# Kernel optimization log

Hardware: AMD Instinct MI355X
Metric: run time of the kernel (lower is better)

The kernel has to match this reference:

```python
import jax, jax.numpy as jnp
import numpy as np

EMBEDDING_SIZE = 50
MAX_DOCUMENT_LENGTH = 100
MAX_LABEL = 15
VOCAB = 200000
HID = 1024
BATCH = 4096


def setup_inputs() -> dict:
    key = jax.random.key(0)
    ks = jax.random.split(key, 8)
    x = jax.random.randint(ks[0], (BATCH, MAX_DOCUMENT_LENGTH), 0, VOCAB)
    emb_table = jax.random.normal(ks[1], (VOCAB, EMBEDDING_SIZE), jnp.float32) * 0.05
    # Keras GRUCell (reset_after=True): kernel [E,3H], recurrent_kernel [H,3H],
    # bias [2,3H] split into input bias and recurrent bias; gate order z, r, h.
    kernel = jax.random.normal(ks[2], (EMBEDDING_SIZE, 3 * HID), jnp.float32) * (1.0 / np.sqrt(EMBEDDING_SIZE))
    rec_kernel = jax.random.normal(ks[3], (HID, 3 * HID), jnp.float32) * (1.0 / np.sqrt(HID))
    bias_i = jnp.zeros((3 * HID,), jnp.float32)
    bias_r = jnp.zeros((3 * HID,), jnp.float32)
    Wd = jax.random.normal(ks[4], (HID, MAX_LABEL), jnp.float32) * (1.0 / np.sqrt(HID))
    bd = jnp.zeros((MAX_LABEL,), jnp.float32)
    return {"x": x, "drop_rate": 0, "emb_table": emb_table, "kernel": kernel,
            "rec_kernel": rec_kernel, "bias_i": bias_i, "bias_r": bias_r,
            "Wd": Wd, "bd": bd}


def _gru_scan(emb, kernel, rec_kernel, bias_i, bias_r):
    # emb: [B,T,E] -> time-major [T,B,E]
    emb_t = jnp.transpose(emb, (1, 0, 2))
    B = emb.shape[0]
    h0 = jnp.zeros((B, HID), emb.dtype)

    def step(h, x_t):
        xp = x_t @ kernel + bias_i            # [B,3H]
        hp = h @ rec_kernel + bias_r          # [B,3H]
        xz, xr, xh = jnp.split(xp, 3, axis=-1)
        hz, hr, hh = jnp.split(hp, 3, axis=-1)
        z = jax.nn.sigmoid(xz + hz)
        r = jax.nn.sigmoid(xr + hr)
        hcand = jnp.tanh(xh + r * hh)
        h_new = z * h + (1.0 - z) * hcand
        return h_new, None

    h_last, _ = jax.lax.scan(step, h0, emb_t)
    return h_last


def reference(x, drop_rate, emb_table, kernel, rec_kernel, bias_i, bias_r, Wd, bd):
    emb = emb_table[x]                         # [B,T,E]
    encoding = _gru_scan(emb, kernel, rec_kernel, bias_i, bias_r)  # [B,H]
    if drop_rate > 0:                          # drop_rate is a static Python int
        keep = 1.0 - float(drop_rate)
        mask = jax.random.bernoulli(jax.random.key(1), keep, encoding.shape)
        encoding = jnp.where(mask, encoding / keep, 0.0)
    logits = encoding @ Wd + bd                # [B,15]
    return logits
```

## Files before the change

kernel.cpp:

```cpp
#include <hip/hip_runtime.h>
#include <stdint.h>

#define H_DIM   1024
#define G3      3072
#define EMB     50
#define TSTEPS  100
#define NB      4096
#define NLABEL  15

typedef __bf16 bf16x8 __attribute__((ext_vector_type(8)));
typedef float  f32x4  __attribute__((ext_vector_type(4)));
typedef int    i32x4  __attribute__((ext_vector_type(4)));

__device__ inline uint16_t f2bf(float f) {
  uint32_t u = __builtin_bit_cast(uint32_t, f);
  u += 0x7FFFu + ((u >> 16) & 1u);
  return (uint16_t)(u >> 16);
}

__device__ inline void gld16(const void* g, void* l) {
  __builtin_amdgcn_global_load_lds(
      (const __attribute__((address_space(1))) uint32_t*)g,
      (__attribute__((address_space(3))) uint32_t*)l, 16, 0, 0);
}

#define VM(n) do { asm volatile("s_waitcnt vmcnt(" #n ")" ::: "memory"); \
                   __builtin_amdgcn_sched_barrier(0); } while (0)
#define LGKM0() do { asm volatile("s_waitcnt lgkmcnt(0)" ::: "memory"); \
                     __builtin_amdgcn_sched_barrier(0); } while (0)
#define BARF() do { __builtin_amdgcn_s_barrier(); \
                    asm volatile("" ::: "memory"); } while (0)
#define GLDB(dst, addr, OFF) \
  asm volatile("global_load_dwordx4 %0, %1, off offset:" OFF \
               : "=&v"(dst) : "v"(addr) : "memory")


__global__ __launch_bounds__(256) void prep_recT(const float* __restrict__ rec,
                                                 uint16_t* __restrict__ recT) {
  __shared__ uint16_t st[64][72];
  const int n0 = blockIdx.x * 64;
  const int k0 = blockIdx.y * 64;
  const int tid = threadIdx.x;
#pragma unroll
  for (int i = 0; i < 16; ++i) {
    int idx = tid + i * 256;
    int r = idx >> 6;
    int c = idx & 63;
    st[c][r] = f2bf(rec[(size_t)(k0 + r) * G3 + n0 + c]);
  }
  __syncthreads();
#pragma unroll
  for (int i = 0; i < 16; ++i) {
    int idx = tid + i * 256;
    int r = idx >> 6;
    int c = idx & 63;
    recT[(size_t)(n0 + r) * H_DIM + k0 + c] = st[r][c];
  }
}

__global__ __launch_bounds__(256) void prep_kerT(const float* __restrict__ ker,
                                                 uint16_t* __restrict__ kerT) {
  int n = blockIdx.x * 4 + (threadIdx.x >> 6);
  int k = threadIdx.x & 63;
  float v = (k < EMB) ? ker[(size_t)k * G3 + n] : 0.f;
  kerT[(size_t)n * 64 + k] = f2bf(v);
}

__global__ __launch_bounds__(256) void prep_pack(const uint16_t* __restrict__ recT,
                                                 const uint16_t* __restrict__ kerT,
                                                 uint16_t* __restrict__ Bpk) {
  int cid = blockIdx.x * 256 + threadIdx.x;
  int lane = cid & 63;
  int r = cid >> 6;
  int ks = r & 1; r >>= 1;
  int nf = r & 1; r >>= 1;
  int wn = r & 1; r >>= 1;
  int g  = r % 3; r /= 3;
  int kt = r % 17;
  int colblk = r / 17;
  int n  = g * H_DIM + colblk * 64 + wn * 32 + nf * 16 + (lane & 15);
  int kk = ks * 32 + (lane >> 4) * 8;
  const uint16_t* src = (kt < 16) ? recT + (size_t)n * H_DIM + kt * 64 + kk
                                  : kerT + (size_t)n * 64 + kk;
  *reinterpret_cast<i32x4*>(Bpk + (size_t)cid * 8) =
      *reinterpret_cast<const i32x4*>(src);
}

__global__ __launch_bounds__(256) void prep_embt(const int* __restrict__ x,
                                                 const float* __restrict__ tab,
                                                 uint16_t* __restrict__ embt) {
  int idx = blockIdx.x * 256 + threadIdx.x;
  int g = idx >> 5;
  int p = idx & 31;
  int t = g >> 12;
  int b = g & 4095;
  int row = x[b * TSTEPS + t];
  float2 v;
  if (p < 25) v = *reinterpret_cast<const float2*>(tab + (size_t)row * EMB + 2 * p);
  else { v.x = 0.f; v.y = 0.f; }
  uint32_t packed = (uint32_t)f2bf(v.x) | ((uint32_t)f2bf(v.y) << 16);
  *reinterpret_cast<uint32_t*>(embt + (size_t)g * 64 + 2 * p) = packed;
}

__global__ __launch_bounds__(256, 2) void gru_step_kernel(
    const uint16_t* __restrict__ hb_prev,
    float* __restrict__ hf,
    uint16_t* __restrict__ hb_next,
    const uint16_t* __restrict__ Bpk,
    const uint16_t* __restrict__ embt,
    const float* __restrict__ bias_i,
    const float* __restrict__ bias_r) {
  __shared__ __align__(16) uint16_t sA2[2][128 * 64];

  const int tid  = threadIdx.x;
  const int lane = tid & 63;
  const int wid  = tid >> 6;
  const int wm   = wid >> 1;
  const int wn   = wid & 1;
  const int bid  = blockIdx.x;
  const int xk = bid & 7, slot = bid >> 3;
  const int rowblk = (xk >> 1) * 8 + (slot >> 3);
  const int colblk = (xk & 1) * 8 + (slot & 7);
  const int r0 = rowblk * 128;
  const int j0 = colblk * 64;

  const int swz8 = 8 * ((lane & 7) ^ (lane >> 3));

  bf16x8 af[4][2];
  i32x4  bfv[3][2][2];
  f32x4 accZ[4][2], accR[4][2], accH[4][2], accX[4][2];
#pragma unroll
  for (int m = 0; m < 4; ++m)
#pragma unroll
    for (int n = 0; n < 2; ++n) {
      accZ[m][n] = (f32x4){0.f, 0.f, 0.f, 0.f};
      accR[m][n] = (f32x4){0.f, 0.f, 0.f, 0.f};
      accH[m][n] = (f32x4){0.f, 0.f, 0.f, 0.f};
      accX[m][n] = (f32x4){0.f, 0.f, 0.f, 0.f};
    }

  const uint16_t* pB[3];
#pragma unroll
  for (int g = 0; g < 3; ++g)
    pB[g] = Bpk + (size_t)colblk * 17 * 12288 + g * 4096 + wn * 2048 + lane * 8;

  auto stageA = [&](int t) {
    const int abuf = t & 1;
#pragma unroll
    for (int i = 0; i < 4; ++i) {
      int chunk = wid * 4 + i;
      int row = chunk * 8 + (lane >> 3);
      const uint16_t* src = (t < 16)
          ? hb_prev + (size_t)(r0 + row) * H_DIM + t * 64 + swz8
          : embt + (size_t)(r0 + row) * 64 + swz8;
      gld16(src, &sA2[abuf][(chunk * 64 + lane) * 8]);
    }
  };
  auto readA = [&](int t) {
    const int abuf = t & 1;
#pragma unroll
    for (int ks = 0; ks < 2; ++ks) {
      const int colswz = (ks * 32 + (lane >> 4) * 8) ^ ((lane & 7) << 3);
#pragma unroll
      for (int mf = 0; mf < 4; ++mf)
        af[mf][ks] = *reinterpret_cast<const bf16x8*>(
            &sA2[abuf][(wm * 64 + mf * 16 + (lane & 15)) * 64 + colswz]);
    }
  };

#define ISSUE_BG(g) do { \
    GLDB(bfv[g][0][0], pB[g], "0");    GLDB(bfv[g][0][1], pB[g], "1024"); \
    GLDB(bfv[g][1][0], pB[g], "2048"); GLDB(bfv[g][1][1], pB[g], "3072"); \
  } while (0)
#define MFG(g, ACC) do { \
    __builtin_amdgcn_s_setprio(1); \
    _Pragma("unroll") for (int ks = 0; ks < 2; ++ks) \
    _Pragma("unroll") for (int nf = 0; nf < 2; ++nf) \
    _Pragma("unroll") for (int mf = 0; mf < 4; ++mf) \
      ACC[mf][nf] = __builtin_amdgcn_mfma_f32_16x16x32_bf16( \
          af[mf][ks], __builtin_bit_cast(bf16x8, bfv[g][nf][ks]), \
          ACC[mf][nf], 0, 0, 0); \
    __builtin_amdgcn_s_setprio(0); \
  } while (0)
#define ADV_B() do { _Pragma("unroll") \
    for (int g = 0; g < 3; ++g) pB[g] += 12288; } while (0)

  stageA(0); stageA(1);
  ISSUE_BG(0); ISSUE_BG(1); ISSUE_BG(2);
  ADV_B();
  VM(12);
  BARF();
  readA(0);

  for (int t = 0; t < 15; ++t) {
    stageA(t + 2);
    VM(12);
    MFG(0, accZ); ISSUE_BG(0);
    VM(12);
    MFG(1, accR); ISSUE_BG(1);
    VM(12);
    MFG(2, accH); ISSUE_BG(2);
    ADV_B();
    readA(t + 1);
    LGKM0();
    VM(12);
    BARF();
  }

  VM(8);  MFG(0, accZ); ISSUE_BG(0);
  VM(8);  MFG(1, accR); ISSUE_BG(1);
  VM(8);  MFG(2, accH); ISSUE_BG(2);
  readA(16);
  LGKM0();
  VM(8);  MFG(0, accZ);
  VM(4);  MFG(1, accR);
  VM(0);  MFG(2, accX);

#undef ISSUE_BG
#undef MFG
#undef ADV_B

#pragma unroll
  for (int nf = 0; nf < 2; ++nf) {
    int col = j0 + wn * 32 + nf * 16 + (lane & 15);
    float b_z = bias_i[col] + bias_r[col];
    float b_r = bias_i[H_DIM + col] + bias_r[H_DIM + col];
    float bih = bias_i[2 * H_DIM + col];
    float brh = bias_r[2 * H_DIM + col];
#pragma unroll
    for (int mf = 0; mf < 4; ++mf) {
#pragma unroll
      for (int q = 0; q < 4; ++q) {
        int row = r0 + wm * 64 + mf * 16 + (lane >> 4) * 4 + q;
        float z  = 1.f / (1.f + __expf(-(accZ[mf][nf][q] + b_z)));
        float rr = 1.f / (1.f + __expf(-(accR[mf][nf][q] + b_r)));
        float pre = accX[mf][nf][q] + bih + rr * (accH[mf][nf][q] + brh);
        float hc  = 2.f / (1.f + __expf(-2.f * pre)) - 1.f;
        size_t idx = (size_t)row * H_DIM + col;
        float hold = hf[idx];
        float hnew = z * hold + (1.f - z) * hc;
        hf[idx] = hnew;
        hb_next[idx] = f2bf(hnew);
      }
    }
  }
}

__global__ __launch_bounds__(64) void logits_kernel(const float* __restrict__ hf,
                                                    const float* __restrict__ Wd,
                                                    const float* __restrict__ bd,
                                                    float* __restrict__ out) {
  int b = blockIdx.x;
  int l = threadIdx.x;
  float p[NLABEL];
#pragma unroll
  for (int o = 0; o < NLABEL; ++o) p[o] = 0.f;
  for (int kb = 0; kb < 16; ++kb) {
    int k = kb * 64 + l;
    float hv = hf[(size_t)b * H_DIM + k];
#pragma unroll
    for (int o = 0; o < NLABEL; ++o) p[o] += hv * Wd[k * NLABEL + o];
  }
#pragma unroll
  for (int o = 0; o < NLABEL; ++o) {
#pragma unroll
    for (int s = 32; s; s >>= 1) p[o] += __shfl_xor(p[o], s);
  }
  if (l == 0) {
#pragma unroll
    for (int o = 0; o < NLABEL; ++o) out[(size_t)b * NLABEL + o] = p[o] + bd[o];
  }
}

extern "C" void kernel_launch(void* const* d_in, const int* in_sizes, int n_in,
                              void* d_out, int out_size, void* d_ws, size_t ws_size,
                              hipStream_t stream) {
  const int*   x          = (const int*)d_in[0];
  const float* emb_table  = (const float*)d_in[2];
  const float* kernel_w   = (const float*)d_in[3];
  const float* rec_kernel = (const float*)d_in[4];
  const float* bias_i     = (const float*)d_in[5];
  const float* bias_r     = (const float*)d_in[6];
  const float* Wd         = (const float*)d_in[7];
  const float* bd         = (const float*)d_in[8];
  float* out = (float*)d_out;

  char* ws = (char*)d_ws;
  size_t off = 0;
  auto alloc = [&](size_t bytes) {
    char* p = ws + off;
    off += (bytes + 255) & ~(size_t)255;
    return p;
  };
  float*    hf   = (float*)alloc((size_t)NB * H_DIM * 4);
  uint16_t* hb0  = (uint16_t*)alloc((size_t)NB * H_DIM * 2);
  uint16_t* hb1  = (uint16_t*)alloc((size_t)NB * H_DIM * 2);
  uint16_t* recT = (uint16_t*)alloc((size_t)G3 * H_DIM * 2);
  uint16_t* kerT = (uint16_t*)alloc((size_t)G3 * 64 * 2);
  uint16_t* embt = (uint16_t*)alloc((size_t)TSTEPS * NB * 64 * 2);
  uint16_t* Bpk  = (uint16_t*)alloc((size_t)16 * 17 * 12288 * 2);
  if (off > ws_size) return;

  hipMemsetAsync(hf, 0, (size_t)NB * H_DIM * 4, stream);
  hipMemsetAsync(hb0, 0, (size_t)NB * H_DIM * 2, stream);

  prep_recT<<<dim3(G3 / 64, H_DIM / 64), 256, 0, stream>>>(rec_kernel, recT);
  prep_kerT<<<G3 / 4, 256, 0, stream>>>(kernel_w, kerT);
  prep_pack<<<1632, 256, 0, stream>>>(recT, kerT, Bpk);
  prep_embt<<<TSTEPS * NB * 32 / 256, 256, 0, stream>>>(x, emb_table, embt);

  uint16_t* hb[2] = {hb0, hb1};
  for (int t = 0; t < TSTEPS; ++t) {
    gru_step_kernel<<<512, 256, 0, stream>>>(
        hb[t & 1], hf, hb[(t + 1) & 1], Bpk,
        embt + (size_t)t * NB * 64, bias_i, bias_r);
  }
  logits_kernel<<<NB, 64, 0, stream>>>(hf, Wd, bd, out);
}
```

Baseline: 3.151 ms.

## Deepen GRU step pipeline to triple-buffered A tiles and double-buffered B registers

Moves the per-step GEMM loop from a two-stage LDS ring for the hidden/embedding A tiles to a three-stage ring. It also alternates between two register sets for the recurrent-kernel B fragments, so B loads are issued two K-tiles ahead. The per-gate vmcnt waits inside the tile are removed in favour of one wait per tile, meant to hide global-load latency behind MFMA work. The cost is 50% more LDS and roughly double the B-fragment registers. With launch_bounds(256,2) this risks spills or lower occupancy, and the reworked wait counts risk consuming data before it has arrived.

```diff
diff --git a/kernel.cpp b/kernel.cpp
--- a/kernel.cpp
+++ b/kernel.cpp
@@ -110,7 +110,7 @@
     const uint16_t* __restrict__ embt,
     const float* __restrict__ bias_i,
     const float* __restrict__ bias_r) {
-  __shared__ __align__(16) uint16_t sA2[2][128 * 64];
+  __shared__ __align__(16) uint16_t sA[3][128 * 64];
 
   const int tid  = threadIdx.x;
   const int lane = tid & 63;
@@ -127,7 +127,7 @@
   const int swz8 = 8 * ((lane & 7) ^ (lane >> 3));
 
   bf16x8 af[4][2];
-  i32x4  bfv[3][2][2];
+  i32x4  bfvA[3][2][2], bfvB[3][2][2];
   f32x4 accZ[4][2], accR[4][2], accH[4][2], accX[4][2];
 #pragma unroll
   for (int m = 0; m < 4; ++m)
@@ -145,7 +145,7 @@
     pB[g] = Bpk + (size_t)colblk * 17 * 12288 + g * 4096 + wn * 2048 + lane * 8;
 
   auto stageA = [&](int t) {
-    const int abuf = t & 1;
+    int ab = t % 3;
 #pragma unroll
     for (int i = 0; i < 4; ++i) {
       int chunk = wid * 4 + i;
@@ -153,72 +153,78 @@
       const uint16_t* src = (t < 16)
           ? hb_prev + (size_t)(r0 + row) * H_DIM + t * 64 + swz8
           : embt + (size_t)(r0 + row) * 64 + swz8;
-      gld16(src, &sA2[abuf][(chunk * 64 + lane) * 8]);
+      gld16(src, &sA[ab][(chunk * 64 + lane) * 8]);
     }
   };
   auto readA = [&](int t) {
-    const int abuf = t & 1;
+    int ab = t % 3;
 #pragma unroll
     for (int ks = 0; ks < 2; ++ks) {
       const int colswz = (ks * 32 + (lane >> 4) * 8) ^ ((lane & 7) << 3);
 #pragma unroll
       for (int mf = 0; mf < 4; ++mf)
         af[mf][ks] = *reinterpret_cast<const bf16x8*>(
-            &sA2[abuf][(wm * 64 + mf * 16 + (lane & 15)) * 64 + colswz]);
+            &sA[ab][(wm * 64 + mf * 16 + (lane & 15)) * 64 + colswz]);
     }
   };
 
-#define ISSUE_BG(g) do { \
-    GLDB(bfv[g][0][0], pB[g], "0");    GLDB(bfv[g][0][1], pB[g], "1024"); \
-    GLDB(bfv[g][1][0], pB[g], "2048"); GLDB(bfv[g][1][1], pB[g], "3072"); \
+#define ISSUE_BG(g, BF) do { \
+    GLDB(BF[g][0][0], pB[g], "0");    GLDB(BF[g][0][1], pB[g], "1024"); \
+    GLDB(BF[g][1][0], pB[g], "2048"); GLDB(BF[g][1][1], pB[g], "3072"); \
   } while (0)
-#define MFG(g, ACC) do { \
+#define MFG(g, BF, ACC) do { \
     __builtin_amdgcn_s_setprio(1); \
     _Pragma("unroll") for (int ks = 0; ks < 2; ++ks) \
     _Pragma("unroll") for (int nf = 0; nf < 2; ++nf) \
     _Pragma("unroll") for (int mf = 0; mf < 4; ++mf) \
       ACC[mf][nf] = __builtin_amdgcn_mfma_f32_16x16x32_bf16( \
-          af[mf][ks], __builtin_bit_cast(bf16x8, bfv[g][nf][ks]), \
+          af[mf][ks], __builtin_bit_cast(bf16x8, BF[g][nf][ks]), \
           ACC[mf][nf], 0, 0, 0); \
     __builtin_amdgcn_s_setprio(0); \
   } while (0)
 #define ADV_B() do { _Pragma("unroll") \
     for (int g = 0; g < 3; ++g) pB[g] += 12288; } while (0)
 
-  stageA(0); stageA(1);
-  ISSUE_BG(0); ISSUE_BG(1); ISSUE_BG(2);
-  ADV_B();
+#define TILE_STEADY(t, BF) do { \
+    stageA((t) + 3); \
+    MFG(0, BF, accZ); ISSUE_BG(0, BF); \
+    MFG(1, BF, accR); ISSUE_BG(1, BF); \
+    MFG(2, BF, accH); ISSUE_BG(2, BF); ADV_B(); \
+    readA((t) + 1); LGKM0(); \
+    VM(16); BARF(); \
+  } while (0)
+
+  stageA(0); stageA(1); stageA(2);
+  ISSUE_BG(0, bfvA); ISSUE_BG(1, bfvA); ISSUE_BG(2, bfvA); ADV_B();
+  ISSUE_BG(0, bfvB); ISSUE_BG(1, bfvB); ISSUE_BG(2, bfvB); ADV_B();
   VM(12);
   BARF();
   readA(0);
 
-  for (int t = 0; t < 15; ++t) {
-    stageA(t + 2);
-    VM(12);
-    MFG(0, accZ); ISSUE_BG(0);
-    VM(12);
-    MFG(1, accR); ISSUE_BG(1);
-    VM(12);
-    MFG(2, accH); ISSUE_BG(2);
-    ADV_B();
-    readA(t + 1);
-    LGKM0();
-    VM(12);
-    BARF();
-  }
-
-  VM(8);  MFG(0, accZ); ISSUE_BG(0);
-  VM(8);  MFG(1, accR); ISSUE_BG(1);
-  VM(8);  MFG(2, accH); ISSUE_BG(2);
-  readA(16);
-  LGKM0();
-  VM(8);  MFG(0, accZ);
-  VM(4);  MFG(1, accR);
-  VM(0);  MFG(2, accX);
+  for (int tt = 0; tt < 14; tt += 2) {
+    TILE_STEADY(tt, bfvA);
+    TILE_STEADY(tt + 1, bfvB);
+  }
+
+  MFG(0, bfvA, accZ); ISSUE_BG(0, bfvA);
+  MFG(1, bfvA, accR); ISSUE_BG(1, bfvA);
+  MFG(2, bfvA, accH); ISSUE_BG(2, bfvA);
+  readA(15); LGKM0();
+  VM(12);
+  BARF();
+  MFG(0, bfvB, accZ);
+  MFG(1, bfvB, accR);
+  MFG(2, bfvB, accH);
+  readA(16); LGKM0();
+  VM(0);
+  MFG(0, bfvA, accZ);
+  MFG(1, bfvA, accR);
+  MFG(2, bfvA, accX);
 
 #undef ISSUE_BG
 #undef MFG
 #undef ADV_B
+#undef TILE_STEADY
 
 #pragma unroll
   for (int nf = 0; nf < 2; ++nf) {
```

After: 4.985 ms. +58.2%, slower.

## Stage recurrent weight tiles through double-buffered LDS instead of direct register loads

Applied to the files above, without the earlier changes.

The GRU step kernel used to load the packed recurrent/input weight fragments straight from global memory into registers with inline-asm dwordx4 loads, interleaved per gate with the MFMAs. It now stages each k-tile of B (12288 bf16) into a double-buffered LDS array using global_load_lds, then reads fragments from LDS alongside the A tile. This restructures the pipeline into a barrier-synchronised stage/compute/read loop. It adds 48KB of LDS per block, which may reduce occupancy at 2 blocks per CU, plus an extra barrier per iteration. It also removes the per-gate overlap of loads with compute.

```diff
diff --git a/kernel.cpp b/kernel.cpp
--- a/kernel.cpp
+++ b/kernel.cpp
@@ -30,9 +30,6 @@
                      __builtin_amdgcn_sched_barrier(0); } while (0)
 #define BARF() do { __builtin_amdgcn_s_barrier(); \
                     asm volatile("" ::: "memory"); } while (0)
-#define GLDB(dst, addr, OFF) \
-  asm volatile("global_load_dwordx4 %0, %1, off offset:" OFF \
-               : "=&v"(dst) : "v"(addr) : "memory")
 
 
 __global__ __launch_bounds__(256) void prep_recT(const float* __restrict__ rec,
@@ -111,6 +108,7 @@
     const float* __restrict__ bias_i,
     const float* __restrict__ bias_r) {
   __shared__ __align__(16) uint16_t sA2[2][128 * 64];
+  __shared__ __align__(16) uint16_t sB2[2][12288];
 
   const int tid  = threadIdx.x;
   const int lane = tid & 63;
@@ -126,8 +124,10 @@
 
   const int swz8 = 8 * ((lane & 7) ^ (lane >> 3));
 
+  const uint16_t* pBcol = Bpk + (size_t)colblk * 17 * 12288;
+
   bf16x8 af[4][2];
-  i32x4  bfv[3][2][2];
+  bf16x8 bfr[3][2][2];
   f32x4 accZ[4][2], accR[4][2], accH[4][2], accX[4][2];
 #pragma unroll
   for (int m = 0; m < 4; ++m)
@@ -138,11 +138,6 @@
       accH[m][n] = (f32x4){0.f, 0.f, 0.f, 0.f};
       accX[m][n] = (f32x4){0.f, 0.f, 0.f, 0.f};
     }
-
-  const uint16_t* pB[3];
-#pragma unroll
-  for (int g = 0; g < 3; ++g)
-    pB[g] = Bpk + (size_t)colblk * 17 * 12288 + g * 4096 + wn * 2048 + lane * 8;
 
   auto stageA = [&](int t) {
     const int abuf = t & 1;
@@ -156,6 +151,15 @@
       gld16(src, &sA2[abuf][(chunk * 64 + lane) * 8]);
     }
   };
+  auto stageB = [&](int t) {
+    const int bbuf = t & 1;
+    const uint16_t* base = pBcol + (size_t)t * 12288;
+#pragma unroll
+    for (int i = 0; i < 6; ++i) {
+      int e = (i * 256 + tid) * 8;
+      gld16(base + e, &sB2[bbuf][e]);
+    }
+  };
   auto readA = [&](int t) {
     const int abuf = t & 1;
 #pragma unroll
@@ -167,58 +171,61 @@
             &sA2[abuf][(wm * 64 + mf * 16 + (lane & 15)) * 64 + colswz]);
     }
   };
-
-#define ISSUE_BG(g) do { \
-    GLDB(bfv[g][0][0], pB[g], "0");    GLDB(bfv[g][0][1], pB[g], "1024"); \
-    GLDB(bfv[g][1][0], pB[g], "2048"); GLDB(bfv[g][1][1], pB[g], "3072"); \
-  } while (0)
+  auto readB = [&](int t) {
+    const int bbuf = t & 1;
+#pragma unroll
+    for (int g = 0; g < 3; ++g)
+#pragma unroll
+      for (int nf = 0; nf < 2; ++nf)
+#pragma unroll
+        for (int ks = 0; ks < 2; ++ks) {
+          int c = g * 8 + wn * 4 + nf * 2 + ks;
+          bfr[g][nf][ks] = *reinterpret_cast<const bf16x8*>(
+              &sB2[bbuf][c * 512 + lane * 8]);
+        }
+  };
+
 #define MFG(g, ACC) do { \
     __builtin_amdgcn_s_setprio(1); \
     _Pragma("unroll") for (int ks = 0; ks < 2; ++ks) \
     _Pragma("unroll") for (int nf = 0; nf < 2; ++nf) \
     _Pragma("unroll") for (int mf = 0; mf < 4; ++mf) \
       ACC[mf][nf] = __builtin_amdgcn_mfma_f32_16x16x32_bf16( \
-          af[mf][ks], __builtin_bit_cast(bf16x8, bfv[g][nf][ks]), \
-          ACC[mf][nf], 0, 0, 0); \
+          af[mf][ks], bfr[g][nf][ks], ACC[mf][nf], 0, 0, 0); \
     __builtin_amdgcn_s_setprio(0); \
   } while (0)
-#define ADV_B() do { _Pragma("unroll") \
-    for (int g = 0; g < 3; ++g) pB[g] += 12288; } while (0)
-
-  stageA(0); stageA(1);
-  ISSUE_BG(0); ISSUE_BG(1); ISSUE_BG(2);
-  ADV_B();
-  VM(12);
+
+  stageA(0); stageB(0);
+  stageA(1); stageB(1);
+  VM(10);
   BARF();
-  readA(0);
+  readA(0); readB(0);
+  LGKM0();
 
   for (int t = 0; t < 15; ++t) {
-    stageA(t + 2);
-    VM(12);
-    MFG(0, accZ); ISSUE_BG(0);
-    VM(12);
-    MFG(1, accR); ISSUE_BG(1);
-    VM(12);
-    MFG(2, accH); ISSUE_BG(2);
-    ADV_B();
-    readA(t + 1);
+    BARF();
+    stageA(t + 2); stageB(t + 2);
+    MFG(0, accZ);
+    MFG(1, accR);
+    MFG(2, accH);
+    VM(10);
+    BARF();
+    readA(t + 1); readB(t + 1);
     LGKM0();
-    VM(12);
-    BARF();
-  }
-
-  VM(8);  MFG(0, accZ); ISSUE_BG(0);
-  VM(8);  MFG(1, accR); ISSUE_BG(1);
-  VM(8);  MFG(2, accH); ISSUE_BG(2);
-  readA(16);
+  }
+
+  MFG(0, accZ);
+  MFG(1, accR);
+  MFG(2, accH);
+  VM(0);
+  BARF();
+  readA(16); readB(16);
   LGKM0();
-  VM(8);  MFG(0, accZ);
-  VM(4);  MFG(1, accR);
-  VM(0);  MFG(2, accX);
-
-#undef ISSUE_BG
+  MFG(0, accZ);
+  MFG(1, accR);
+  MFG(2, accX);
+
 #undef MFG
-#undef ADV_B
 
 #pragma unroll
   for (int nf = 0; nf < 2; ++nf) {
```

Measured after the change: 3.134 ms. No clear change (-0.6%).
